# Kernel tuning notes

Hardware: AMD Instinct MI355X
Metric: run time of the kernel (lower is better)

The kernel has to match this reference:

```python
import jax, jax.numpy as jnp
import numpy as np

B, S, H = 2, 2048, 896
NH, NKV, HD = 14, 2, 64        # heads, kv heads, head_dim
GROUPS = NH // NKV             # 7
ROPE_THETA = 1000000.0


def rotate_half(x):
    x1 = x[..., : x.shape[-1] // 2]
    x2 = x[..., x.shape[-1] // 2:]
    return jnp.concatenate([-x2, x1], axis=-1)


def rope_tables(seq_len):
    inv_freq = 1.0 / ROPE_THETA ** (jnp.arange(0, HD, 2, dtype=jnp.float32) / HD)
    t = jnp.arange(seq_len, dtype=jnp.float32)
    freqs = jnp.outer(t, inv_freq)            # [S, HD/2]
    emb = jnp.concatenate([freqs, freqs], -1)  # [S, HD]
    return jnp.cos(emb), jnp.sin(emb)


def setup_inputs() -> dict:
    key = jax.random.key(0)
    ks = jax.random.split(key, 8)
    sc = 0.02
    hidden_states = jax.random.normal(ks[0], (B, S, H), jnp.float32)
    causal = jnp.tril(jnp.ones((S, S), jnp.bool_))
    attention_mask = jnp.where(causal, 0.0, -1e9).astype(jnp.float32)[None, None]
    return {
        "hidden_states": hidden_states,
        "attention_mask": attention_mask,
        "Wq": jax.random.normal(ks[1], (H, NH * HD), jnp.float32) * sc,
        "bq": jnp.zeros((NH * HD,), jnp.float32),
        "Wk": jax.random.normal(ks[2], (H, NKV * HD), jnp.float32) * sc,
        "bk": jnp.zeros((NKV * HD,), jnp.float32),
        "Wv": jax.random.normal(ks[3], (H, NKV * HD), jnp.float32) * sc,
        "bv": jnp.zeros((NKV * HD,), jnp.float32),
        "Wo": jax.random.normal(ks[4], (H, H), jnp.float32) * sc,
    }


def reference(hidden_states, attention_mask, Wq, bq, Wk, bk, Wv, bv, Wo):
    b, s, _ = hidden_states.shape
    q = (hidden_states @ Wq + bq).reshape(b, s, NH, HD).transpose(0, 2, 1, 3)   # [b,nh,s,hd]
    k = (hidden_states @ Wk + bk).reshape(b, s, NKV, HD).transpose(0, 2, 1, 3)  # [b,nkv,s,hd]
    v = (hidden_states @ Wv + bv).reshape(b, s, NKV, HD).transpose(0, 2, 1, 3)
    cos, sin = rope_tables(s)                 # position_offset = 0
    cos = cos[None, None]; sin = sin[None, None]
    q = q * cos + rotate_half(q) * sin
    k = k * cos + rotate_half(k) * sin
    # GQA: expand kv heads to full heads (matches jnp.repeat on axis=1)
    k = jnp.repeat(k, GROUPS, axis=1)
    v = jnp.repeat(v, GROUPS, axis=1)
    scores = jnp.einsum('bhqd,bhkd->bhqk', q, k) / np.sqrt(HD).astype(np.float32)
    scores = scores + attention_mask
    attn = jax.nn.softmax(scores, axis=-1)
    out = jnp.einsum('bhqk,bhkd->bhqd', attn, v)
    out = out.transpose(0, 2, 1, 3).reshape(b, s, NH * HD)
    return out @ Wo
```

## Files before the change

### kernel.cpp

```cpp
#include <hip/hip_runtime.h>

#define S_LEN 2048
#define NHEADS 14
#define NKVH 2
#define HDIM 64
#define HID 896
#define NQKV 1152
#define NCHUNK 40

typedef __bf16 bf16;
typedef __bf16 bf16x4 __attribute__((ext_vector_type(4)));
typedef __bf16 bf16x8 __attribute__((ext_vector_type(8)));
typedef float f32x4 __attribute__((ext_vector_type(4)));
typedef unsigned int u32x4 __attribute__((ext_vector_type(4)));

__device__ inline f32x4 mfma16(bf16x8 a, bf16x8 b, f32x4 c) {
  return __builtin_amdgcn_mfma_f32_16x16x32_bf16(a, b, c, 0, 0, 0);
}

__device__ inline void gload_lds16(const bf16* g, bf16* l) {
  __builtin_amdgcn_global_load_lds(
      (const __attribute__((address_space(1))) void*)g,
      (__attribute__((address_space(3))) void*)l, 16, 0, 0);
}
__device__ inline void gload_lds16b(const void* g, void* l) {
  __builtin_amdgcn_global_load_lds(
      (const __attribute__((address_space(1))) void*)g,
      (__attribute__((address_space(3))) void*)l, 16, 0, 0);
}

__device__ inline unsigned cvtpk(float lo, float hi) {
  unsigned r;
  asm("v_cvt_pk_bf16_f32 %0, %1, %2" : "=v"(r) : "v"(lo), "v"(hi));
  return r;
}

__device__ inline void chunk_map(int c, int& qt, int& ch) {
  if (c < 4)       { qt = c;                ch = 0; }
  else if (c < 12) { qt = 4 + ((c - 4) >> 1); ch = (c - 4) & 1; }
  else if (c < 24) { int d = c - 12; qt = 8 + d / 3; ch = d % 3; }
  else             { int d = c - 24; qt = 12 + (d >> 2); ch = d & 3; }
}

__global__ __launch_bounds__(256) void prep_kernel(
    const float* __restrict__ X, bf16* __restrict__ Xb,
    const float* __restrict__ Wq, const float* __restrict__ Wk,
    const float* __restrict__ Wv, const float* __restrict__ Wo,
    bf16* __restrict__ WqkvT, bf16* __restrict__ WoT,
    const float* __restrict__ bq, const float* __restrict__ bk,
    const float* __restrict__ bv, float* __restrict__ biasq,
    float* __restrict__ trig) {
  __shared__ float tile[32][33];
  int blk = blockIdx.x;
  int tid = threadIdx.x;
  if (blk < 3584) {
    int i = blk * 256 + tid;
    if (i < 917504) {
      float4 v = reinterpret_cast<const float4*>(X)[i];
      bf16x4 o;
      o[0] = (bf16)v.x; o[1] = (bf16)v.y; o[2] = (bf16)v.z; o[3] = (bf16)v.w;
      reinterpret_cast<bf16x4*>(Xb)[i] = o;
    }
    return;
  }
  if (blk < 5376) {
    int t = blk - 3584;
    const float* W; bf16* dst; int N, bx, by;
    if (t < 784)       { W = Wq; dst = WqkvT;                      N = 896; bx = t % 28;          by = t / 28; }
    else if (t < 896)  { int u = t - 784;  W = Wk; dst = WqkvT + (size_t)896 * 896;  N = 128; bx = u % 4; by = u / 4; }
    else if (t < 1008) { int u = t - 896;  W = Wv; dst = WqkvT + (size_t)1024 * 896; N = 128; bx = u % 4; by = u / 4; }
    else               { int u = t - 1008; W = Wo; dst = WoT;      N = 896; bx = u % 28;          by = u / 28; }
    int n0 = bx * 32, k0 = by * 32;
    int tx = tid & 31, ty = tid >> 5;
#pragma unroll
    for (int j = 0; j < 32; j += 8)
      tile[ty + j][tx] = W[(size_t)(k0 + ty + j) * N + n0 + tx];
    __syncthreads();
#pragma unroll
    for (int j = 0; j < 32; j += 8)
      dst[(size_t)(n0 + ty + j) * HID + k0 + tx] = (bf16)tile[tx][ty + j];
    return;
  }
  if (blk < 5381) {
    int i = (blk - 5376) * 256 + tid;
    if (i < 896) biasq[i] = bq[i];
    else if (i < 1024) biasq[i] = bk[i - 896];
    else if (i < 1152) biasq[i] = bv[i - 1024];
    return;
  }
  {
    int ti = blk - 5381;
    int s = ti * 8 + (tid >> 5);
    int d = tid & 31;
    float inv = expf(-(float)d * (13.815510557964274f / 32.0f));
    float a = (float)s * inv;
    float c, si;
    sincosf(a, &si, &c);
    trig[(size_t)s * 64 + d] = c;
    trig[(size_t)s * 64 + 32 + d] = si;
  }
}

__global__ __launch_bounds__(256) void gemm_qkv_kernel(const bf16* __restrict__ A,
                                                       const bf16* __restrict__ Bt,
                                                       const float* __restrict__ bias,
                                                       const float* __restrict__ trig,
                                                       bf16* __restrict__ Qb,
                                                       bf16* __restrict__ Kb,
                                                       bf16* __restrict__ Vt) {
  __shared__ __align__(16) char smem[33280];
  bf16* As = (bf16*)smem;
  bf16* Bs = (bf16*)(smem + 16384);
  float* tileO = (float*)smem;
  const int K = 896;
  int n0 = blockIdx.x * 64, m0 = blockIdx.y * 128;
  int tid = threadIdx.x;
  int wid = tid >> 6, lane = tid & 63;
  int lr = lane & 15, lh = lane >> 4;
  int wr = wid >> 1, wc = wid & 1;
  f32x4 acc[4][2] = {};

  auto stage = [&](int buf, int k0) {
#pragma unroll
    for (int i = 0; i < 2; ++i) {
      int seg = i * 4 + wid;
      int idx = seg * 512 + lane * 8;
      int r = idx >> 5, c = idx & 31;
      gload_lds16(A + (size_t)(m0 + r) * K + k0 + c, As + buf * 4096 + seg * 512);
    }
    {
      int idx = wid * 512 + lane * 8;
      int r = idx >> 5, c = idx & 31;
      gload_lds16(Bt + (size_t)(n0 + r) * K + k0 + c, Bs + buf * 2048 + wid * 512);
    }
  };

  stage(0, 0);
  __syncthreads();
  int nk = K >> 5;
  int cur = 0;
  for (int t = 0; t < nk; ++t) {
    if (t + 1 < nk) stage(cur ^ 1, (t + 1) << 5);
    bf16x8 am[4], bn[2];
#pragma unroll
    for (int mf = 0; mf < 4; ++mf)
      am[mf] = *reinterpret_cast<const bf16x8*>(As + cur * 4096 + (wr * 64 + mf * 16 + lr) * 32 + lh * 8);
#pragma unroll
    for (int nf = 0; nf < 2; ++nf)
      bn[nf] = *reinterpret_cast<const bf16x8*>(Bs + cur * 2048 + (wc * 32 + nf * 16 + lr) * 32 + lh * 8);
    __builtin_amdgcn_s_setprio(1);
#pragma unroll
    for (int mf = 0; mf < 4; ++mf)
#pragma unroll
      for (int nf = 0; nf < 2; ++nf)
        acc[mf][nf] = mfma16(am[mf], bn[nf], acc[mf][nf]);
    __builtin_amdgcn_s_setprio(0);
    __syncthreads();
    cur ^= 1;
  }

#pragma unroll
  for (int nf = 0; nf < 2; ++nf) {
    int col = wc * 32 + nf * 16 + lr;
    float bb = bias[n0 + col];
#pragma unroll
    for (int mf = 0; mf < 4; ++mf) {
      int row0 = wr * 64 + mf * 16 + lh * 4;
#pragma unroll
      for (int j = 0; j < 4; ++j)
        tileO[(row0 + j) * 65 + col] = acc[mf][nf][j] + bb;
    }
  }
  __syncthreads();

  const float QSCALE = 0.125f * 1.44269504088896f;
  int b = blockIdx.y >> 4;
  int s0 = (blockIdx.y & 15) * 128;
  int bx = blockIdx.x;
  if (bx < 14) {
    int r2 = tid >> 1, half = tid & 1;
    int s = s0 + r2;
    const float* tr = trig + (size_t)s * 64;
    size_t base = ((size_t)(b * NHEADS + bx) * S_LEN + s) * HDIM;
    bf16x8 o1[2], o2[2];
#pragma unroll
    for (int v = 0; v < 2; ++v)
#pragma unroll
      for (int p = 0; p < 8; ++p) {
        int d = half * 16 + v * 8 + p;
        float c = tr[d], sn = tr[32 + d];
        float v1 = tileO[r2 * 65 + d], v2 = tileO[r2 * 65 + d + 32];
        o1[v][p] = (bf16)((v1 * c - v2 * sn) * QSCALE);
        o2[v][p] = (bf16)((v2 * c + v1 * sn) * QSCALE);
      }
    *(bf16x8*)(Qb + base + half * 16)      = o1[0];
    *(bf16x8*)(Qb + base + half * 16 + 8)  = o1[1];
    *(bf16x8*)(Qb + base + 32 + half * 16)     = o2[0];
    *(bf16x8*)(Qb + base + 32 + half * 16 + 8) = o2[1];
  } else if (bx < 16) {
    int kh = bx - 14;
    int r2 = tid >> 1, half = tid & 1;
    int s = s0 + r2;
    const float* tr = trig + (size_t)s * 64;
    int sw = (((s & 7) ^ ((s >> 3) & 1)) << 3);
    size_t base = ((size_t)(b * NKVH + kh) * S_LEN + s) * HDIM;
#pragma unroll
    for (int p = 0; p < 16; ++p) {
      int d = half * 16 + p;
      float c = tr[d], sn = tr[32 + d];
      float v1 = tileO[r2 * 65 + d], v2 = tileO[r2 * 65 + d + 32];
      Kb[base + (d ^ sw)]        = (bf16)(v1 * c - v2 * sn);
      Kb[base + ((d + 32) ^ sw)] = (bf16)(v2 * c + v1 * sn);
    }
  } else {
    int kh = bx - 16;
    int d = tid & 63, seg = tid >> 6;
    size_t vbase = ((size_t)(b * NKVH + kh) * HDIM + d) * S_LEN;
    int c8 = (d & 7) << 3;
#pragma unroll
    for (int g = 0; g < 4; ++g) {
      int sl = seg * 32 + g * 8;
      bf16x8 w;
#pragma unroll
      for (int p = 0; p < 8; ++p)
        w[p] = (bf16)tileO[(sl + p) * 65 + d];
      int s = s0 + sl;
      int col = (s & ~63) | (((s & 63) ^ c8) & ~7);
      *(bf16x8*)(Vt + vbase + col) = w;
    }
  }
}

__global__ __launch_bounds__(256) void gemm_bt_kernel(const bf16* __restrict__ A,
                                                      const bf16* __restrict__ Bt,
                                                      float* __restrict__ C,
                                                      int M, int N, int K) {
  __shared__ __align__(16) bf16 As[2][128][32];
  __shared__ __align__(16) bf16 Bs[2][64][32];
  int n0 = blockIdx.x * 64, m0 = blockIdx.y * 128;
  int tid = threadIdx.x;
  int wid = tid >> 6, lane = tid & 63;
  int lr = lane & 15, lh = lane >> 4;
  int wr = wid >> 1, wc = wid & 1;
  f32x4 acc[4][2] = {};

  auto stage = [&](int buf, int k0) {
#pragma unroll
    for (int i = 0; i < 2; ++i) {
      int seg = i * 4 + wid;
      int idx = seg * 512 + lane * 8;
      int r = idx >> 5, c = idx & 31;
      gload_lds16(A + (size_t)(m0 + r) * K + k0 + c, &As[buf][0][0] + seg * 512);
    }
    {
      int idx = wid * 512 + lane * 8;
      int r = idx >> 5, c = idx & 31;
      gload_lds16(Bt + (size_t)(n0 + r) * K + k0 + c, &Bs[buf][0][0] + wid * 512);
    }
  };

  stage(0, 0);
  __syncthreads();
  int nk = K >> 5;
  int cur = 0;
  for (int t = 0; t < nk; ++t) {
    if (t + 1 < nk) stage(cur ^ 1, (t + 1) << 5);
    bf16x8 am[4], bn[2];
#pragma unroll
    for (int mf = 0; mf < 4; ++mf)
      am[mf] = *reinterpret_cast<const bf16x8*>(&As[cur][wr * 64 + mf * 16 + lr][lh * 8]);
#pragma unroll
    for (int nf = 0; nf < 2; ++nf)
      bn[nf] = *reinterpret_cast<const bf16x8*>(&Bs[cur][wc * 32 + nf * 16 + lr][lh * 8]);
    __builtin_amdgcn_s_setprio(1);
#pragma unroll
    for (int mf = 0; mf < 4; ++mf)
#pragma unroll
      for (int nf = 0; nf < 2; ++nf)
        acc[mf][nf] = mfma16(am[mf], bn[nf], acc[mf][nf]);
    __builtin_amdgcn_s_setprio(0);
    __syncthreads();
    cur ^= 1;
  }

#pragma unroll
  for (int nf = 0; nf < 2; ++nf) {
    int col = n0 + wc * 32 + nf * 16 + lr;
#pragma unroll
    for (int mf = 0; mf < 4; ++mf) {
      int row0 = m0 + wr * 64 + mf * 16 + lh * 4;
#pragma unroll
      for (int j = 0; j < 4; ++j)
        C[(size_t)(row0 + j) * N + col] = acc[mf][nf][j];
    }
  }
}

__global__ __launch_bounds__(256, 4) void attn_kernel(const bf16* __restrict__ Qb,
                                                      const bf16* __restrict__ Kb,
                                                      const bf16* __restrict__ Vt,
                                                      bf16* __restrict__ Opart,
                                                      float* __restrict__ Oml) {
  int blk = blockIdx.x;
  int c = (NCHUNK - 1) - (blk % NCHUNK), bh = blk / NCHUNK;
  int qt, ch;
  chunk_map(c, qt, ch);
  int h = bh % NHEADS, b = bh / NHEADS;
  int q0 = qt * 128;
  int kv = h / 7;
  int kc0 = ch * 512;
  int kend = min(kc0 + 512, q0 + 128);
  int nt = (kend - kc0) >> 6;
  int tid = threadIdx.x, wid = tid >> 6, lane = tid & 63;
  int lr = lane & 15, lh = lane >> 4;
  int swk = (lr & 7) << 4;

  const bf16* Qp = Qb + ((size_t)(b * NHEADS + h) * S_LEN + q0 + wid * 32) * HDIM;
  const char* KpB = (const char*)(Kb + (size_t)(b * NKVH + kv) * S_LEN * HDIM);
  const char* VpB = (const char*)(Vt + (size_t)(b * NKVH + kv) * HDIM * S_LEN);

  __shared__ __align__(16) bf16 Ks[2][4096];
  __shared__ __align__(16) bf16 Vs[2][4096];

  bf16x8 aq[2][2];
#pragma unroll
  for (int f = 0; f < 2; ++f)
#pragma unroll
    for (int kk = 0; kk < 2; ++kk)
      aq[f][kk] = *reinterpret_cast<const bf16x8*>(
          Qp + (size_t)(f * 16 + lr) * HDIM + kk * 32 + lh * 8);

  float m[2] = {-3.0e38f, -3.0e38f}, l[2] = {0.f, 0.f};
  f32x4 o[2][4] = {};

  auto stage = [&](int buf, int kv0) {
#pragma unroll
    for (int i = 0; i < 2; ++i) {
      gload_lds16b(KpB + (size_t)kv0 * 128 + wid * 2048 + i * 1024 + lane * 16,
                   &Ks[buf][wid * 1024 + i * 512]);
      int d = wid * 16 + i * 8 + (lane >> 3);
      gload_lds16b(VpB + (size_t)d * (S_LEN * 2) + kv0 * 2 + (lane & 7) * 16,
                   &Vs[buf][wid * 1024 + i * 512]);
    }
  };

  stage(0, kc0);
  __syncthreads();

  int qf0 = q0 + wid * 32;
  int cur = 0;
  for (int t = 0; t < nt; ++t) {
    int kv0 = kc0 + (t << 6);
    const char* KsB = (const char*)&Ks[cur][0];
    f32x4 sacc[2][4] = {};
#pragma unroll
    for (int nf = 0; nf < 4; ++nf) {
      int rowk = 8 * (lr >> 2) + (lr & 3) + ((nf & 1) << 2) + ((nf >> 1) << 5);
      int rsw = (((rowk & 7) ^ ((rowk >> 3) & 1)) << 4);
#pragma unroll
      for (int kk = 0; kk < 2; ++kk) {
        bf16x8 kb = *(const bf16x8*)(KsB + rowk * 128 + ((kk * 64 + lh * 16) ^ rsw));
        sacc[0][nf] = mfma16(kb, aq[0][kk], sacc[0][nf]);
        sacc[1][nf] = mfma16(kb, aq[1][kk], sacc[1][nf]);
      }
    }
    if (t + 1 < nt) stage(cur ^ 1, kv0 + 64);

    float mx[2];
#pragma unroll
    for (int f = 0; f < 2; ++f) {
      int qg = qf0 + f * 16 + lr;
      if (kv0 + 63 > qf0 + f * 16) {
#pragma unroll
        for (int nf = 0; nf < 4; ++nf) {
          int kb0 = kv0 + ((nf & 1) << 2) + ((nf >> 1) << 5) + (lh << 3);
#pragma unroll
          for (int j = 0; j < 4; ++j)
            if (kb0 + j > qg) sacc[f][nf][j] = -3.0e38f;
        }
      }
      f32x4 m4 = sacc[f][0];
#pragma unroll
      for (int nf = 1; nf < 4; ++nf)
#pragma unroll
        for (int j = 0; j < 4; ++j) m4[j] = fmaxf(m4[j], sacc[f][nf][j]);
      float mxl = fmaxf(fmaxf(m4[0], m4[1]), fmaxf(m4[2], m4[3]));
      mxl = fmaxf(mxl, __shfl_xor(mxl, 16));
      mxl = fmaxf(mxl, __shfl_xor(mxl, 32));
      mx[f] = mxl;
    }
    float g = fmaxf(mx[0] - m[0], mx[1] - m[1]);
    if (!__all(g <= 8.0f)) {
#pragma unroll
      for (int f = 0; f < 2; ++f) {
        float mn = fmaxf(m[f], mx[f]);
        float al = exp2f(m[f] - mn);
        m[f] = mn;
        l[f] *= al;
        f32x4 av;
#pragma unroll
        for (int j = 0; j < 4; ++j) av[j] = __shfl(al, (lh << 2) + j);
#pragma unroll
        for (int nf = 0; nf < 4; ++nf) o[f][nf] *= av;
      }
    }
    bf16x8 pa[2][2];
#pragma unroll
    for (int f = 0; f < 2; ++f) {
      f32x4 rs4 = {0.f, 0.f, 0.f, 0.f};
#pragma unroll
      for (int nf = 0; nf < 4; ++nf) {
#pragma unroll
        for (int j = 0; j < 4; ++j)
          sacc[f][nf][j] = exp2f(sacc[f][nf][j] - m[f]);
        rs4 += sacc[f][nf];
      }
      float rsum = (rs4[0] + rs4[1]) + (rs4[2] + rs4[3]);
      rsum += __shfl_xor(rsum, 16);
      rsum += __shfl_xor(rsum, 32);
      l[f] += rsum;
#pragma unroll
      for (int kk = 0; kk < 2; ++kk) {
        u32x4 w;
        w[0] = cvtpk(sacc[f][2 * kk][0], sacc[f][2 * kk][1]);
        w[1] = cvtpk(sacc[f][2 * kk][2], sacc[f][2 * kk][3]);
        w[2] = cvtpk(sacc[f][2 * kk + 1][0], sacc[f][2 * kk + 1][1]);
        w[3] = cvtpk(sacc[f][2 * kk + 1][2], sacc[f][2 * kk + 1][3]);
        pa[f][kk] = __builtin_bit_cast(bf16x8, w);
      }
    }
    const char* VsB = (const char*)&Vs[cur][0];
#pragma unroll
    for (int nf = 0; nf < 4; ++nf) {
#pragma unroll
      for (int kk = 0; kk < 2; ++kk) {
        bf16x8 vb = *(const bf16x8*)(VsB + (nf * 16 + lr) * 128 + ((kk * 64 + lh * 16) ^ swk));
        o[0][nf] = mfma16(pa[0][kk], vb, o[0][nf]);
        o[1][nf] = mfma16(pa[1][kk], vb, o[1][nf]);
      }
    }
    __syncthreads();
    cur ^= 1;
  }

  size_t pbase = ((size_t)bh * NCHUNK + c) * (128 * 64);
#pragma unroll
  for (int f = 0; f < 2; ++f)
#pragma unroll
    for (int nf = 0; nf < 4; ++nf) {
      int col = nf * 16 + lr;
#pragma unroll
      for (int j = 0; j < 4; ++j) {
        int rloc = wid * 32 + f * 16 + (lh << 2) + j;
        Opart[pbase + (size_t)rloc * 64 + col] = (bf16)o[f][nf][j];
      }
    }
  if (lane < 16) {
    size_t mbase = ((size_t)bh * NCHUNK + c) * 128;
#pragma unroll
    for (int f = 0; f < 2; ++f) {
      int rloc = wid * 32 + f * 16 + lane;
      Oml[(mbase + rloc) * 2]     = m[f];
      Oml[(mbase + rloc) * 2 + 1] = l[f];
    }
  }
}

__global__ __launch_bounds__(256) void combine_kernel(const bf16* __restrict__ Opart,
                                                      const float* __restrict__ Oml,
                                                      bf16* __restrict__ Ob) {
  int blk = blockIdx.x;
  int qt = blk & 15, bh = blk >> 4;
  int h = bh % NHEADS, b = bh / NHEADS;
  int a = qt >> 2, bb = qt & 3;
  int nch = a + 1;
  int coff = (a + 1) * (2 * a + bb);
  int t = threadIdx.x;
  int row = t >> 1, cg = t & 1;

  float M = -__builtin_inff();
  for (int i = 0; i < nch; ++i)
    M = fmaxf(M, Oml[(((size_t)bh * NCHUNK + coff + i) * 128 + row) * 2]);
  float L = 0.f;
  for (int i = 0; i < nch; ++i) {
    size_t mb = (((size_t)bh * NCHUNK + coff + i) * 128 + row) * 2;
    L += exp2f(Oml[mb] - M) * Oml[mb + 1];
  }
  float acc[32];
#pragma unroll
  for (int k = 0; k < 32; ++k) acc[k] = 0.f;
  for (int i = 0; i < nch; ++i) {
    size_t mb = (((size_t)bh * NCHUNK + coff + i) * 128 + row) * 2;
    float w = exp2f(Oml[mb] - M);
    const bf16* src = Opart + (((size_t)bh * NCHUNK + coff + i) * 128 + row) * 64 + cg * 32;
#pragma unroll
    for (int v = 0; v < 4; ++v) {
      bf16x8 x = *reinterpret_cast<const bf16x8*>(src + v * 8);
#pragma unroll
      for (int k = 0; k < 8; ++k) acc[v * 8 + k] += w * (float)x[k];
    }
  }
  float inv = 1.0f / L;
  bf16* dst = Ob + ((size_t)(b * S_LEN) + qt * 128 + row) * HID + h * 64 + cg * 32;
#pragma unroll
  for (int v = 0; v < 4; ++v) {
    bf16x8 r;
#pragma unroll
    for (int k = 0; k < 8; ++k) r[k] = (bf16)(acc[v * 8 + k] * inv);
    *reinterpret_cast<bf16x8*>(dst + v * 8) = r;
  }
}

extern "C" void kernel_launch(void* const* d_in, const int* in_sizes, int n_in,
                              void* d_out, int out_size, void* d_ws, size_t ws_size,
                              hipStream_t stream) {
  (void)in_sizes; (void)n_in; (void)out_size; (void)ws_size;
  const float* X  = (const float*)d_in[0];
  const float* Wq = (const float*)d_in[2];
  const float* bq = (const float*)d_in[3];
  const float* Wk = (const float*)d_in[4];
  const float* bk = (const float*)d_in[5];
  const float* Wv = (const float*)d_in[6];
  const float* bv = (const float*)d_in[7];
  const float* Wo = (const float*)d_in[8];
  float* OUT = (float*)d_out;

  char* ws = (char*)d_ws;
  bf16*  Xb    = (bf16*)(ws);
  bf16*  WqkvT = (bf16*)(ws + 7340032);
  bf16*  WoT   = (bf16*)(ws + 9404416);
  float* biasq = (float*)(ws + 11010048);
  bf16*  Opart = (bf16*)(ws + 11014656);
  float* trig  = (float*)(ws + 29364736);
  bf16*  Qbuf  = (bf16*)(ws + 29889024);
  bf16*  Kbuf  = (bf16*)(ws + 37229056);
  bf16*  Vbuf  = (bf16*)(ws + 38277632);
  float* Oml   = (float*)(ws + 7340032);
  bf16*  Obuf  = Xb;

  prep_kernel<<<5637, 256, 0, stream>>>(X, Xb, Wq, Wk, Wv, Wo, WqkvT, WoT,
                                        bq, bk, bv, biasq, trig);
  gemm_qkv_kernel<<<dim3(18, 32), 256, 0, stream>>>(Xb, WqkvT, biasq, trig,
                                                    Qbuf, Kbuf, Vbuf);
  attn_kernel<<<28 * NCHUNK, 256, 0, stream>>>(Qbuf, Kbuf, Vbuf, Opart, Oml);
  combine_kernel<<<28 * 16, 256, 0, stream>>>(Opart, Oml, Obuf);
  gemm_bt_kernel<<<dim3(14, 32), 256, 0, stream>>>(Obuf, WoT, OUT, 4096, 896, 896);
}
```

Before: 106.8 us.

## Widen attention query tile to 256 rows with 8 waves per block

Doubles the attention block's query tile from 128 to 256 rows, running 8 waves per block, and halves the number of KV chunks so each staged K/V tile serves twice as many queries. Each wave now stages a single 16-byte slice, and the combine kernel indexing is updated for the 256-row partials. The launch order of chunks is also changed from reverse to forward. This cuts redundant K/V loads and partial-output traffic but gives fewer blocks, more causal waste in diagonal tiles, and possible tail imbalance.

```diff
diff --git a/kernel.cpp b/kernel.cpp
--- a/kernel.cpp
+++ b/kernel.cpp
@@ -6,7 +6,7 @@
 #define HDIM 64
 #define HID 896
 #define NQKV 1152
-#define NCHUNK 40
+#define NCHUNK 20
 
 typedef __bf16 bf16;
 typedef __bf16 bf16x4 __attribute__((ext_vector_type(4)));
@@ -36,10 +36,14 @@
 }
 
 __device__ inline void chunk_map(int c, int& qt, int& ch) {
-  if (c < 4)       { qt = c;                ch = 0; }
-  else if (c < 12) { qt = 4 + ((c - 4) >> 1); ch = (c - 4) & 1; }
-  else if (c < 24) { int d = c - 12; qt = 8 + d / 3; ch = d % 3; }
-  else             { int d = c - 24; qt = 12 + (d >> 2); ch = d & 3; }
+  if (c < 1)       { qt = 0; ch = 0; }
+  else if (c < 2)  { qt = 1; ch = 0; }
+  else if (c < 4)  { qt = 2; ch = c - 2; }
+  else if (c < 6)  { qt = 3; ch = c - 4; }
+  else if (c < 9)  { qt = 4; ch = c - 6; }
+  else if (c < 12) { qt = 5; ch = c - 9; }
+  else if (c < 16) { qt = 6; ch = c - 12; }
+  else             { qt = 7; ch = c - 16; }
 }
 
 __global__ __launch_bounds__(256) void prep_kernel(
@@ -296,20 +300,20 @@
   }
 }
 
-__global__ __launch_bounds__(256, 4) void attn_kernel(const bf16* __restrict__ Qb,
+__global__ __launch_bounds__(512, 4) void attn_kernel(const bf16* __restrict__ Qb,
                                                       const bf16* __restrict__ Kb,
                                                       const bf16* __restrict__ Vt,
                                                       bf16* __restrict__ Opart,
                                                       float* __restrict__ Oml) {
   int blk = blockIdx.x;
-  int c = (NCHUNK - 1) - (blk % NCHUNK), bh = blk / NCHUNK;
+  int c = blk % NCHUNK, bh = blk / NCHUNK;
   int qt, ch;
   chunk_map(c, qt, ch);
   int h = bh % NHEADS, b = bh / NHEADS;
-  int q0 = qt * 128;
+  int q0 = qt * 256;
   int kv = h / 7;
   int kc0 = ch * 512;
-  int kend = min(kc0 + 512, q0 + 128);
+  int kend = min(kc0 + 512, q0 + 256);
   int nt = (kend - kc0) >> 6;
   int tid = threadIdx.x, wid = tid >> 6, lane = tid & 63;
   int lr = lane & 15, lh = lane >> 4;
@@ -334,14 +338,11 @@
   f32x4 o[2][4] = {};
 
   auto stage = [&](int buf, int kv0) {
-#pragma unroll
-    for (int i = 0; i < 2; ++i) {
-      gload_lds16b(KpB + (size_t)kv0 * 128 + wid * 2048 + i * 1024 + lane * 16,
-                   &Ks[buf][wid * 1024 + i * 512]);
-      int d = wid * 16 + i * 8 + (lane >> 3);
-      gload_lds16b(VpB + (size_t)d * (S_LEN * 2) + kv0 * 2 + (lane & 7) * 16,
-                   &Vs[buf][wid * 1024 + i * 512]);
-    }
+    gload_lds16b(KpB + (size_t)kv0 * 128 + wid * 1024 + lane * 16,
+                 &Ks[buf][wid * 512]);
+    int d = wid * 8 + (lane >> 3);
+    gload_lds16b(VpB + (size_t)d * (S_LEN * 2) + kv0 * 2 + (lane & 7) * 16,
+                 &Vs[buf][wid * 512]);
   };
 
   stage(0, kc0);
@@ -443,7 +444,7 @@
     cur ^= 1;
   }
 
-  size_t pbase = ((size_t)bh * NCHUNK + c) * (128 * 64);
+  size_t pbase = ((size_t)bh * NCHUNK + c) * (256 * 64);
 #pragma unroll
   for (int f = 0; f < 2; ++f)
 #pragma unroll
@@ -456,7 +457,7 @@
       }
     }
   if (lane < 16) {
-    size_t mbase = ((size_t)bh * NCHUNK + c) * 128;
+    size_t mbase = ((size_t)bh * NCHUNK + c) * 256;
 #pragma unroll
     for (int f = 0; f < 2; ++f) {
       int rloc = wid * 32 + f * 16 + lane;
@@ -470,29 +471,30 @@
                                                       const float* __restrict__ Oml,
                                                       bf16* __restrict__ Ob) {
   int blk = blockIdx.x;
-  int qt = blk & 15, bh = blk >> 4;
+  int sub = blk & 15, bh = blk >> 4;
+  int qt = sub >> 1, half = sub & 1;
   int h = bh % NHEADS, b = bh / NHEADS;
-  int a = qt >> 2, bb = qt & 3;
+  int a = qt >> 1, b2 = qt & 1;
   int nch = a + 1;
-  int coff = (a + 1) * (2 * a + bb);
+  int coff = (a + 1) * (a + b2);
   int t = threadIdx.x;
-  int row = t >> 1, cg = t & 1;
+  int row = half * 128 + (t >> 1), cg = t & 1;
 
   float M = -__builtin_inff();
   for (int i = 0; i < nch; ++i)
-    M = fmaxf(M, Oml[(((size_t)bh * NCHUNK + coff + i) * 128 + row) * 2]);
+    M = fmaxf(M, Oml[(((size_t)bh * NCHUNK + coff + i) * 256 + row) * 2]);
   float L = 0.f;
   for (int i = 0; i < nch; ++i) {
-    size_t mb = (((size_t)bh * NCHUNK + coff + i) * 128 + row) * 2;
+    size_t mb = (((size_t)bh * NCHUNK + coff + i) * 256 + row) * 2;
     L += exp2f(Oml[mb] - M) * Oml[mb + 1];
   }
   float acc[32];
 #pragma unroll
   for (int k = 0; k < 32; ++k) acc[k] = 0.f;
   for (int i = 0; i < nch; ++i) {
-    size_t mb = (((size_t)bh * NCHUNK + coff + i) * 128 + row) * 2;
+    size_t mb = (((size_t)bh * NCHUNK + coff + i) * 256 + row) * 2;
     float w = exp2f(Oml[mb] - M);
-    const bf16* src = Opart + (((size_t)bh * NCHUNK + coff + i) * 128 + row) * 64 + cg * 32;
+    const bf16* src = Opart + (((size_t)bh * NCHUNK + coff + i) * 256 + row) * 64 + cg * 32;
 #pragma unroll
     for (int v = 0; v < 4; ++v) {
       bf16x8 x = *reinterpret_cast<const bf16x8*>(src + v * 8);
@@ -501,7 +503,7 @@
     }
   }
   float inv = 1.0f / L;
-  bf16* dst = Ob + ((size_t)(b * S_LEN) + qt * 128 + row) * HID + h * 64 + cg * 32;
+  bf16* dst = Ob + ((size_t)(b * S_LEN) + qt * 256 + row) * HID + h * 64 + cg * 32;
 #pragma unroll
   for (int v = 0; v < 4; ++v) {
     bf16x8 r;
@@ -542,7 +544,7 @@
                                         bq, bk, bv, biasq, trig);
   gemm_qkv_kernel<<<dim3(18, 32), 256, 0, stream>>>(Xb, WqkvT, biasq, trig,
                                                     Qbuf, Kbuf, Vbuf);
-  attn_kernel<<<28 * NCHUNK, 256, 0, stream>>>(Qbuf, Kbuf, Vbuf, Opart, Oml);
+  attn_kernel<<<28 * NCHUNK, 512, 0, stream>>>(Qbuf, Kbuf, Vbuf, Opart, Oml);
   combine_kernel<<<28 * 16, 256, 0, stream>>>(Opart, Oml, Obuf);
   gemm_bt_kernel<<<dim3(14, 32), 256, 0, stream>>>(Obuf, WoT, OUT, 4096, 896, 896);
 }
```

New measurement: 111.6 us. 4.5% more time.

## Write single-chunk attention tiles directly and reorder chunk scheduling

Applied to the files above, without the earlier changes.

For query tiles covered by a single KV chunk (qt<4), the attention kernel now normalizes its output by l and writes bf16 straight into the final output buffer. This skips the partial-output and m/l stores and shrinks the combine grid to the remaining 12 tiles per head. A lookup table also replaces the reversed chunk index, so heavy chunks are dispatched first and light ones spread out to balance load. The cost is an extra branch and table load in the attention kernel, plus a dependence on the exact chunk-to-tile mapping.

```diff
diff --git a/kernel.cpp b/kernel.cpp
--- a/kernel.cpp
+++ b/kernel.cpp
@@ -41,6 +41,14 @@
   else if (c < 24) { int d = c - 12; qt = 8 + d / 3; ch = d % 3; }
   else             { int d = c - 24; qt = 12 + (d >> 2); ch = d & 3; }
 }
+
+__device__ const int chunk_order[NCHUNK] = {
+  36, 37, 38, 39, 32, 33, 34, 28, 29, 30, 24, 25, 26, 21, 22, 23,
+  18, 19, 15, 16, 12, 13, 10, 11, 8, 6, 4, 3,
+  35, 20, 9, 2,
+  31, 17, 7, 1,
+  27, 14, 5, 0
+};
 
 __global__ __launch_bounds__(256) void prep_kernel(
     const float* __restrict__ X, bf16* __restrict__ Xb,
@@ -300,9 +308,10 @@
                                                       const bf16* __restrict__ Kb,
                                                       const bf16* __restrict__ Vt,
                                                       bf16* __restrict__ Opart,
-                                                      float* __restrict__ Oml) {
+                                                      float* __restrict__ Oml,
+                                                      bf16* __restrict__ Ob) {
   int blk = blockIdx.x;
-  int c = (NCHUNK - 1) - (blk % NCHUNK), bh = blk / NCHUNK;
+  int c = chunk_order[blk % NCHUNK], bh = blk / NCHUNK;
   int qt, ch;
   chunk_map(c, qt, ch);
   int h = bh % NHEADS, b = bh / NHEADS;
@@ -443,6 +452,26 @@
     cur ^= 1;
   }
 
+  if (qt < 4) {
+#pragma unroll
+    for (int f = 0; f < 2; ++f) {
+      f32x4 inv4;
+#pragma unroll
+      for (int j = 0; j < 4; ++j)
+        inv4[j] = 1.0f / __shfl(l[f], (lh << 2) + j);
+#pragma unroll
+      for (int nf = 0; nf < 4; ++nf) {
+        int col = h * 64 + nf * 16 + lr;
+#pragma unroll
+        for (int j = 0; j < 4; ++j) {
+          int rloc = wid * 32 + f * 16 + (lh << 2) + j;
+          Ob[((size_t)(b * S_LEN) + q0 + rloc) * HID + col] = (bf16)(o[f][nf][j] * inv4[j]);
+        }
+      }
+    }
+    return;
+  }
+
   size_t pbase = ((size_t)bh * NCHUNK + c) * (128 * 64);
 #pragma unroll
   for (int f = 0; f < 2; ++f)
@@ -470,7 +499,7 @@
                                                       const float* __restrict__ Oml,
                                                       bf16* __restrict__ Ob) {
   int blk = blockIdx.x;
-  int qt = blk & 15, bh = blk >> 4;
+  int qt = 4 + blk % 12, bh = blk / 12;
   int h = bh % NHEADS, b = bh / NHEADS;
   int a = qt >> 2, bb = qt & 3;
   int nch = a + 1;
@@ -542,7 +571,7 @@
                                         bq, bk, bv, biasq, trig);
   gemm_qkv_kernel<<<dim3(18, 32), 256, 0, stream>>>(Xb, WqkvT, biasq, trig,
                                                     Qbuf, Kbuf, Vbuf);
-  attn_kernel<<<28 * NCHUNK, 256, 0, stream>>>(Qbuf, Kbuf, Vbuf, Opart, Oml);
-  combine_kernel<<<28 * 16, 256, 0, stream>>>(Opart, Oml, Obuf);
+  attn_kernel<<<28 * NCHUNK, 256, 0, stream>>>(Qbuf, Kbuf, Vbuf, Opart, Oml, Obuf);
+  combine_kernel<<<28 * 12, 256, 0, stream>>>(Opart, Oml, Obuf);
   gemm_bt_kernel<<<dim3(14, 32), 256, 0, stream>>>(Obuf, WoT, OUT, 4096, 896, 896);
 }
```

Result: faster. 101.3 us (-5.1%).
